# Optimization experiments

Measured on AMD Instinct MI355X. Metric: run time of the kernel, lower is better.

## Reference

```python
import jax, jax.numpy as jnp
import numpy as np

TAU = 1.0
ITERATIONS = 5
NEG = -1e9  # effectively -inf for masked softmax; exp underflows to exactly 0

B, N, M = 128, 512, 512


def setup_inputs() -> dict:
    key = jax.random.key(0)
    k1, k2, k3 = jax.random.split(key, 3)
    logits = jax.random.normal(k1, (B, N, M), dtype=jnp.float32)
    free_agents_num = jax.random.randint(k2, (B,), 0, M, dtype=jnp.int32)
    tasks_num = jax.random.randint(k3, (B,), 0, M, dtype=jnp.int32)
    return {"logits": logits, "free_agents_num": free_agents_num, "tasks_num": tasks_num}


def reference(logits, free_agents_num, tasks_num):
    # step is None in the original default path -> tau = self.tau
    b, n, m = logits.shape
    row_valid = jnp.arange(n)[None, :] < free_agents_num[:, None]  # [B, N]
    col_valid = jnp.arange(m)[None, :] < tasks_num[:, None]        # [B, M]
    mask = row_valid[:, :, None] & col_valid[:, None, :]           # [B, N, M]
    maskf = mask.astype(logits.dtype)

    x = logits / TAU
    for _ in range(ITERATIONS):
        # torch dim=1 on the [na, nt] slice == axis 2 here (over tasks)
        x = jax.nn.softmax(jnp.where(mask, x, NEG), axis=2) * maskf
        # torch dim=0 on the slice == axis 1 here (over agents)
        x = jax.nn.softmax(jnp.where(mask, x, NEG), axis=1) * maskf
    return x
```

## Files before the change

kernel.cpp:

```cpp
#include <hip/hip_runtime.h>

static constexpr int NB = 128;
static constexpr int NN = 512;
static constexpr int NM = 512;
static constexpr int STRIPS = 8;
static constexpr int NTHREADS = 256;
static constexpr int NITER = 5;
static constexpr int PSZ = NB * NM * STRIPS;


__device__ __forceinline__ float wave_sum(float v) {
#pragma unroll
    for (int off = 32; off >= 1; off >>= 1) v += __shfl_xor(v, off, 64);
    return v;
}

__global__ __launch_bounds__(NTHREADS, 4)
void k0_init(const float* __restrict__ logits, const int* __restrict__ nfree,
             const int* __restrict__ ntask, float* __restrict__ X,
             float* __restrict__ part0)
{
    const int b = blockIdx.x & (NB - 1);
    const int s = blockIdx.x >> 7;
    const int na = nfree[b], nt = ntask[b];
    const int tid = threadIdx.x, wv = tid >> 6, lane = tid & 63;
    float* __restrict__ Xb       = X + (size_t)b * NN * NM;
    const float* __restrict__ Lb = logits + (size_t)b * NN * NM;

    __shared__ __align__(16) float red[4][NM];

    const int m0 = lane * 4, m1 = 256 + lane * 4;
    const bool a0 = (m0 < nt), a1 = (m1 < nt);
    float msk[8];
#pragma unroll
    for (int k = 0; k < 8; ++k)
        msk[k] = (((k < 4) ? m0 + k : m1 + k - 4) < nt) ? 1.f : 0.f;

    const int rstart = s + 8 * wv;
    float ca[8];
#pragma unroll
    for (int k = 0; k < 8; ++k) ca[k] = 0.f;

    int r = rstart;
    for (; r < na; r += 32) {
        float e[8];
#pragma unroll
        for (int k = 0; k < 8; ++k) e[k] = 0.f;
        if (a0) {
            const float4 x = *(const float4*)(Lb + (size_t)r * NM + m0);
            e[0] = msk[0] * __expf(x.x); e[1] = msk[1] * __expf(x.y);
            e[2] = msk[2] * __expf(x.z); e[3] = msk[3] * __expf(x.w);
        }
        if (a1) {
            const float4 x = *(const float4*)(Lb + (size_t)r * NM + m1);
            e[4] = msk[4] * __expf(x.x); e[5] = msk[5] * __expf(x.y);
            e[6] = msk[6] * __expf(x.z); e[7] = msk[7] * __expf(x.w);
        }
        const float sum = wave_sum(((e[0] + e[1]) + (e[2] + e[3])) +
                                   ((e[4] + e[5]) + (e[6] + e[7])));
        const float invr = 1.0f / sum;
        float4 o0 = make_float4(0.f, 0.f, 0.f, 0.f), o1 = o0;
        if (a0) {
            o0 = make_float4(msk[0] * __expf(e[0] * invr), msk[1] * __expf(e[1] * invr),
                             msk[2] * __expf(e[2] * invr), msk[3] * __expf(e[3] * invr));
            ca[0] += o0.x; ca[1] += o0.y; ca[2] += o0.z; ca[3] += o0.w;
        }
        if (a1) {
            o1 = make_float4(msk[4] * __expf(e[4] * invr), msk[5] * __expf(e[5] * invr),
                             msk[6] * __expf(e[6] * invr), msk[7] * __expf(e[7] * invr));
            ca[4] += o1.x; ca[5] += o1.y; ca[6] += o1.z; ca[7] += o1.w;
        }
        *(float4*)(Xb + (size_t)r * NM + m0) = o0;
        *(float4*)(Xb + (size_t)r * NM + m1) = o1;
    }
    const float4 z4 = make_float4(0.f, 0.f, 0.f, 0.f);
    for (; r < NN; r += 32) {
        *(float4*)(Xb + (size_t)r * NM + m0) = z4;
        *(float4*)(Xb + (size_t)r * NM + m1) = z4;
    }

    *(float4*)&red[wv][m0] = make_float4(ca[0], ca[1], ca[2], ca[3]);
    *(float4*)&red[wv][m1] = make_float4(ca[4], ca[5], ca[6], ca[7]);
    __syncthreads();
    {
        float* pb = part0 + (size_t)b * NM * STRIPS;
        const int c = tid * 2;
        pb[(size_t)c * STRIPS + s]       = (red[0][c] + red[1][c]) + (red[2][c] + red[3][c]);
        pb[(size_t)(c + 1) * STRIPS + s] = (red[0][c + 1] + red[1][c + 1]) + (red[2][c + 1] + red[3][c + 1]);
    }
}

__global__ __launch_bounds__(NTHREADS, 4)
void k1_cr(const int* __restrict__ nfree, const int* __restrict__ ntask,
           float* __restrict__ X, const float* __restrict__ ps,
           float* __restrict__ pd)
{
    const int b = blockIdx.x & (NB - 1);
    const int s = blockIdx.x >> 7;
    const int na = nfree[b], nt = ntask[b];
    const int tid = threadIdx.x, wv = tid >> 6, lane = tid & 63;
    float* __restrict__ Xb = X + (size_t)b * NN * NM;

    __shared__ __align__(16) float red[4][NM];
    __shared__ __align__(16) float csh[NM];

    const float* psb = ps + (size_t)b * NM * STRIPS;
    {
        const int c = tid * 2;
        const float4* p0 = (const float4*)(psb + (size_t)c * STRIPS);
        float4 u = p0[0], v = p0[1];
        csh[c] = ((u.x + u.y) + (u.z + u.w)) + ((v.x + v.y) + (v.z + v.w));
        const float4* p1 = (const float4*)(psb + (size_t)(c + 1) * STRIPS);
        u = p1[0]; v = p1[1];
        csh[c + 1] = ((u.x + u.y) + (u.z + u.w)) + ((v.x + v.y) + (v.z + v.w));
    }
    __syncthreads();

    const int m0 = lane * 4, m1 = 256 + lane * 4;
    const bool a0 = (m0 < nt), a1 = (m1 < nt);
    float msk[8], inv[8];
#pragma unroll
    for (int k = 0; k < 8; ++k) {
        const int m = (k < 4) ? m0 + k : m1 + k - 4;
        msk[k] = (m < nt) ? 1.f : 0.f;
        inv[k] = (m < nt) ? 1.0f / csh[m] : 0.f;
    }
    const int rstart = s + 8 * wv;
    float cn[8];
#pragma unroll
    for (int k = 0; k < 8; ++k) cn[k] = 0.f;

    for (int r = rstart; r < na; r += 32) {
        float ez[8];
#pragma unroll
        for (int k = 0; k < 8; ++k) ez[k] = 0.f;
        if (a0) {
            const float4 y = *(const float4*)(Xb + (size_t)r * NM + m0);
            ez[0] = msk[0] * __expf(y.x * inv[0]); ez[1] = msk[1] * __expf(y.y * inv[1]);
            ez[2] = msk[2] * __expf(y.z * inv[2]); ez[3] = msk[3] * __expf(y.w * inv[3]);
        }
        if (a1) {
            const float4 y = *(const float4*)(Xb + (size_t)r * NM + m1);
            ez[4] = msk[4] * __expf(y.x * inv[4]); ez[5] = msk[5] * __expf(y.y * inv[5]);
            ez[6] = msk[6] * __expf(y.z * inv[6]); ez[7] = msk[7] * __expf(y.w * inv[7]);
        }
        const float sum = wave_sum(((ez[0] + ez[1]) + (ez[2] + ez[3])) +
                                   ((ez[4] + ez[5]) + (ez[6] + ez[7])));
        const float invr = 1.0f / sum;
        if (a0) {
            const float4 o = make_float4(
                msk[0] * __expf(ez[0] * invr), msk[1] * __expf(ez[1] * invr),
                msk[2] * __expf(ez[2] * invr), msk[3] * __expf(ez[3] * invr));
            *(float4*)(Xb + (size_t)r * NM + m0) = o;
            cn[0] += o.x; cn[1] += o.y; cn[2] += o.z; cn[3] += o.w;
        }
        if (a1) {
            const float4 o = make_float4(
                msk[4] * __expf(ez[4] * invr), msk[5] * __expf(ez[5] * invr),
                msk[6] * __expf(ez[6] * invr), msk[7] * __expf(ez[7] * invr));
            *(float4*)(Xb + (size_t)r * NM + m1) = o;
            cn[4] += o.x; cn[5] += o.y; cn[6] += o.z; cn[7] += o.w;
        }
    }

    *(float4*)&red[wv][m0] = make_float4(cn[0], cn[1], cn[2], cn[3]);
    *(float4*)&red[wv][m1] = make_float4(cn[4], cn[5], cn[6], cn[7]);
    __syncthreads();
    {
        float* pdb = pd + (size_t)b * NM * STRIPS;
        const int c = tid * 2;
        pdb[(size_t)c * STRIPS + s]       = (red[0][c] + red[1][c]) + (red[2][c] + red[3][c]);
        pdb[(size_t)(c + 1) * STRIPS + s] = (red[0][c + 1] + red[1][c + 1]) + (red[2][c + 1] + red[3][c + 1]);
    }
}

__global__ __launch_bounds__(NTHREADS, 4)
void k2_fin(const int* __restrict__ nfree, const int* __restrict__ ntask,
            float* __restrict__ X, const float* __restrict__ ps)
{
    const int b = blockIdx.x & (NB - 1);
    const int s = blockIdx.x >> 7;
    const int na = nfree[b], nt = ntask[b];
    const int tid = threadIdx.x, wv = tid >> 6, lane = tid & 63;
    float* __restrict__ Xb = X + (size_t)b * NN * NM;

    __shared__ __align__(16) float csh[NM];
    const float* psb = ps + (size_t)b * NM * STRIPS;
    {
        const int c = tid * 2;
        const float4* p0 = (const float4*)(psb + (size_t)c * STRIPS);
        float4 u = p0[0], v = p0[1];
        csh[c] = ((u.x + u.y) + (u.z + u.w)) + ((v.x + v.y) + (v.z + v.w));
        const float4* p1 = (const float4*)(psb + (size_t)(c + 1) * STRIPS);
        u = p1[0]; v = p1[1];
        csh[c + 1] = ((u.x + u.y) + (u.z + u.w)) + ((v.x + v.y) + (v.z + v.w));
    }
    __syncthreads();

    const int m0 = lane * 4, m1 = 256 + lane * 4;
    const bool a0 = (m0 < nt), a1 = (m1 < nt);
    float inv[8];
#pragma unroll
    for (int k = 0; k < 8; ++k) {
        const int m = (k < 4) ? m0 + k : m1 + k - 4;
        inv[k] = (m < nt) ? 1.0f / csh[m] : 0.f;
    }
    const int rstart = s + 8 * wv;
    for (int r = rstart; r < na; r += 32) {
        if (a0) {
            const float4 y = *(const float4*)(Xb + (size_t)r * NM + m0);
            *(float4*)(Xb + (size_t)r * NM + m0) =
                make_float4(y.x * inv[0], y.y * inv[1], y.z * inv[2], y.w * inv[3]);
        }
        if (a1) {
            const float4 y = *(const float4*)(Xb + (size_t)r * NM + m1);
            *(float4*)(Xb + (size_t)r * NM + m1) =
                make_float4(y.x * inv[4], y.y * inv[5], y.z * inv[6], y.w * inv[7]);
        }
    }
}

extern "C" void kernel_launch(void* const* d_in, const int* in_sizes, int n_in,
                              void* d_out, int out_size, void* d_ws, size_t ws_size,
                              hipStream_t stream)
{
    (void)in_sizes; (void)n_in; (void)out_size; (void)ws_size;
    const float* logits = (const float*)d_in[0];
    const int* nfree    = (const int*)d_in[1];
    const int* ntask    = (const int*)d_in[2];
    float* X  = (float*)d_out;
    float* p0 = (float*)d_ws;
    float* p1 = p0 + PSZ;

    const dim3 grid(NB * STRIPS), block(NTHREADS);
    hipLaunchKernelGGL(k0_init, grid, block, 0, stream, logits, nfree, ntask, X, p0);
    const float* src = p0;
    float* dst = p1;
    for (int it = 0; it < NITER - 1; ++it) {
        hipLaunchKernelGGL(k1_cr, grid, block, 0, stream, nfree, ntask, X, src, dst);
        const float* t = src; src = dst; dst = (float*)t;
    }
    hipLaunchKernelGGL(k2_fin, grid, block, 0, stream, nfree, ntask, X, src);
}
```

Measured before the change: 351.7 us.

## Fuse all Sinkhorn passes into one cooperative kernel with grid-wide syncs

Merges the init, iterative column/row normalization, and final scaling kernels into a single cooperative launch that uses grid.sync between passes, with fallback to the multi-launch path if co-residency is not possible. The aim is to remove per-launch overhead and inter-kernel gaps. It requires all 1024 blocks to be co-resident, and grid barriers carry their own cost.

```diff
diff --git a/kernel.cpp b/kernel.cpp
--- a/kernel.cpp
+++ b/kernel.cpp
@@ -1,4 +1,7 @@
 #include <hip/hip_runtime.h>
+#include <hip/hip_cooperative_groups.h>
+
+namespace cg = cooperative_groups;
 
 static constexpr int NB = 128;
 static constexpr int NN = 512;
@@ -15,20 +18,11 @@
     return v;
 }
 
-__global__ __launch_bounds__(NTHREADS, 4)
-void k0_init(const float* __restrict__ logits, const int* __restrict__ nfree,
-             const int* __restrict__ ntask, float* __restrict__ X,
-             float* __restrict__ part0)
-{
-    const int b = blockIdx.x & (NB - 1);
-    const int s = blockIdx.x >> 7;
-    const int na = nfree[b], nt = ntask[b];
-    const int tid = threadIdx.x, wv = tid >> 6, lane = tid & 63;
-    float* __restrict__ Xb       = X + (size_t)b * NN * NM;
-    const float* __restrict__ Lb = logits + (size_t)b * NN * NM;
-
-    __shared__ __align__(16) float red[4][NM];
-
+
+__device__ __forceinline__ void body_init(
+    const float* __restrict__ Lb, float* __restrict__ Xb, float* __restrict__ pb,
+    int s, int na, int nt, int tid, int wv, int lane, float (&red)[4][NM])
+{
     const int m0 = lane * 4, m1 = 256 + lane * 4;
     const bool a0 = (m0 < nt), a1 = (m1 < nt);
     float msk[8];
@@ -83,37 +77,30 @@
     *(float4*)&red[wv][m1] = make_float4(ca[4], ca[5], ca[6], ca[7]);
     __syncthreads();
     {
-        float* pb = part0 + (size_t)b * NM * STRIPS;
         const int c = tid * 2;
         pb[(size_t)c * STRIPS + s]       = (red[0][c] + red[1][c]) + (red[2][c] + red[3][c]);
         pb[(size_t)(c + 1) * STRIPS + s] = (red[0][c + 1] + red[1][c + 1]) + (red[2][c + 1] + red[3][c + 1]);
     }
 }
 
-__global__ __launch_bounds__(NTHREADS, 4)
-void k1_cr(const int* __restrict__ nfree, const int* __restrict__ ntask,
-           float* __restrict__ X, const float* __restrict__ ps,
-           float* __restrict__ pd)
-{
-    const int b = blockIdx.x & (NB - 1);
-    const int s = blockIdx.x >> 7;
-    const int na = nfree[b], nt = ntask[b];
-    const int tid = threadIdx.x, wv = tid >> 6, lane = tid & 63;
-    float* __restrict__ Xb = X + (size_t)b * NN * NM;
-
-    __shared__ __align__(16) float red[4][NM];
-    __shared__ __align__(16) float csh[NM];
-
-    const float* psb = ps + (size_t)b * NM * STRIPS;
-    {
-        const int c = tid * 2;
-        const float4* p0 = (const float4*)(psb + (size_t)c * STRIPS);
-        float4 u = p0[0], v = p0[1];
-        csh[c] = ((u.x + u.y) + (u.z + u.w)) + ((v.x + v.y) + (v.z + v.w));
-        const float4* p1 = (const float4*)(psb + (size_t)(c + 1) * STRIPS);
-        u = p1[0]; v = p1[1];
-        csh[c + 1] = ((u.x + u.y) + (u.z + u.w)) + ((v.x + v.y) + (v.z + v.w));
-    }
+__device__ __forceinline__ void gather_colsums(
+    const float* __restrict__ psb, int tid, float (&csh)[NM])
+{
+    const int c = tid * 2;
+    const float4* p0 = (const float4*)(psb + (size_t)c * STRIPS);
+    float4 u = p0[0], v = p0[1];
+    csh[c] = ((u.x + u.y) + (u.z + u.w)) + ((v.x + v.y) + (v.z + v.w));
+    const float4* p1 = (const float4*)(psb + (size_t)(c + 1) * STRIPS);
+    u = p1[0]; v = p1[1];
+    csh[c + 1] = ((u.x + u.y) + (u.z + u.w)) + ((v.x + v.y) + (v.z + v.w));
+}
+
+__device__ __forceinline__ void body_cr(
+    float* __restrict__ Xb, const float* __restrict__ psb, float* __restrict__ pdb,
+    int s, int na, int nt, int tid, int wv, int lane,
+    float (&red)[4][NM], float (&csh)[NM])
+{
+    gather_colsums(psb, tid, csh);
     __syncthreads();
 
     const int m0 = lane * 4, m1 = 256 + lane * 4;
@@ -167,57 +154,107 @@
     *(float4*)&red[wv][m1] = make_float4(cn[4], cn[5], cn[6], cn[7]);
     __syncthreads();
     {
-        float* pdb = pd + (size_t)b * NM * STRIPS;
         const int c = tid * 2;
         pdb[(size_t)c * STRIPS + s]       = (red[0][c] + red[1][c]) + (red[2][c] + red[3][c]);
         pdb[(size_t)(c + 1) * STRIPS + s] = (red[0][c + 1] + red[1][c + 1]) + (red[2][c + 1] + red[3][c + 1]);
     }
 }
 
+__device__ __forceinline__ void body_fin(
+    float* __restrict__ Xb, const float* __restrict__ psb,
+    int s, int na, int nt, int tid, int wv, int lane, float (&csh)[NM])
+{
+    gather_colsums(psb, tid, csh);
+    __syncthreads();
+
+    const int m0 = lane * 4, m1 = 256 + lane * 4;
+    const bool a0 = (m0 < nt), a1 = (m1 < nt);
+    float inv[8];
+#pragma unroll
+    for (int k = 0; k < 8; ++k) {
+        const int m = (k < 4) ? m0 + k : m1 + k - 4;
+        inv[k] = (m < nt) ? 1.0f / csh[m] : 0.f;
+    }
+    const int rstart = s + 8 * wv;
+    for (int r = rstart; r < na; r += 32) {
+        if (a0) {
+            const float4 y = *(const float4*)(Xb + (size_t)r * NM + m0);
+            *(float4*)(Xb + (size_t)r * NM + m0) =
+                make_float4(y.x * inv[0], y.y * inv[1], y.z * inv[2], y.w * inv[3]);
+        }
+        if (a1) {
+            const float4 y = *(const float4*)(Xb + (size_t)r * NM + m1);
+            *(float4*)(Xb + (size_t)r * NM + m1) =
+                make_float4(y.x * inv[4], y.y * inv[5], y.z * inv[6], y.w * inv[7]);
+        }
+    }
+}
+
+
 __global__ __launch_bounds__(NTHREADS, 4)
-void k2_fin(const int* __restrict__ nfree, const int* __restrict__ ntask,
-            float* __restrict__ X, const float* __restrict__ ps)
-{
+void gs_coop(const float* __restrict__ logits, const int* __restrict__ nfree,
+             const int* __restrict__ ntask, float* __restrict__ X,
+             float* __restrict__ part)
+{
+    cg::grid_group grid = cg::this_grid();
     const int b = blockIdx.x & (NB - 1);
     const int s = blockIdx.x >> 7;
     const int na = nfree[b], nt = ntask[b];
     const int tid = threadIdx.x, wv = tid >> 6, lane = tid & 63;
-    float* __restrict__ Xb = X + (size_t)b * NN * NM;
-
+
+    float* __restrict__ Xb       = X + (size_t)b * NN * NM;
+    const float* __restrict__ Lb = logits + (size_t)b * NN * NM;
+    float* const pbase = part + (size_t)b * NM * STRIPS;
+
+    __shared__ __align__(16) float red[4][NM];
     __shared__ __align__(16) float csh[NM];
-    const float* psb = ps + (size_t)b * NM * STRIPS;
-    {
-        const int c = tid * 2;
-        const float4* p0 = (const float4*)(psb + (size_t)c * STRIPS);
-        float4 u = p0[0], v = p0[1];
-        csh[c] = ((u.x + u.y) + (u.z + u.w)) + ((v.x + v.y) + (v.z + v.w));
-        const float4* p1 = (const float4*)(psb + (size_t)(c + 1) * STRIPS);
-        u = p1[0]; v = p1[1];
-        csh[c + 1] = ((u.x + u.y) + (u.z + u.w)) + ((v.x + v.y) + (v.z + v.w));
-    }
-    __syncthreads();
-
-    const int m0 = lane * 4, m1 = 256 + lane * 4;
-    const bool a0 = (m0 < nt), a1 = (m1 < nt);
-    float inv[8];
-#pragma unroll
-    for (int k = 0; k < 8; ++k) {
-        const int m = (k < 4) ? m0 + k : m1 + k - 4;
-        inv[k] = (m < nt) ? 1.0f / csh[m] : 0.f;
-    }
-    const int rstart = s + 8 * wv;
-    for (int r = rstart; r < na; r += 32) {
-        if (a0) {
-            const float4 y = *(const float4*)(Xb + (size_t)r * NM + m0);
-            *(float4*)(Xb + (size_t)r * NM + m0) =
-                make_float4(y.x * inv[0], y.y * inv[1], y.z * inv[2], y.w * inv[3]);
-        }
-        if (a1) {
-            const float4 y = *(const float4*)(Xb + (size_t)r * NM + m1);
-            *(float4*)(Xb + (size_t)r * NM + m1) =
-                make_float4(y.x * inv[4], y.y * inv[5], y.z * inv[6], y.w * inv[7]);
-        }
-    }
+
+    body_init(Lb, Xb, pbase, s, na, nt, tid, wv, lane, red);
+    grid.sync();
+
+    for (int it = 0; it < NITER - 1; ++it) {
+        const float* psb = pbase + ((it & 1) ? PSZ : 0);
+        float* pdb       = pbase + ((it & 1) ? 0 : PSZ);
+        body_cr(Xb, psb, pdb, s, na, nt, tid, wv, lane, red, csh);
+        grid.sync();
+    }
+    body_fin(Xb, pbase, s, na, nt, tid, wv, lane, csh);
+}
+
+
+__global__ __launch_bounds__(NTHREADS, 4)
+void k0_init(const float* __restrict__ logits, const int* __restrict__ nfree,
+             const int* __restrict__ ntask, float* __restrict__ X,
+             float* __restrict__ part0)
+{
+    const int b = blockIdx.x & (NB - 1), s = blockIdx.x >> 7;
+    const int tid = threadIdx.x, wv = tid >> 6, lane = tid & 63;
+    __shared__ __align__(16) float red[4][NM];
+    body_init(logits + (size_t)b * NN * NM, X + (size_t)b * NN * NM,
+              part0 + (size_t)b * NM * STRIPS, s, nfree[b], ntask[b], tid, wv, lane, red);
+}
+
+__global__ __launch_bounds__(NTHREADS, 4)
+void k1_cr(const int* __restrict__ nfree, const int* __restrict__ ntask,
+           float* __restrict__ X, const float* __restrict__ ps, float* __restrict__ pd)
+{
+    const int b = blockIdx.x & (NB - 1), s = blockIdx.x >> 7;
+    const int tid = threadIdx.x, wv = tid >> 6, lane = tid & 63;
+    __shared__ __align__(16) float red[4][NM];
+    __shared__ __align__(16) float csh[NM];
+    body_cr(X + (size_t)b * NN * NM, ps + (size_t)b * NM * STRIPS,
+            pd + (size_t)b * NM * STRIPS, s, nfree[b], ntask[b], tid, wv, lane, red, csh);
+}
+
+__global__ __launch_bounds__(NTHREADS, 4)
+void k2_fin(const int* __restrict__ nfree, const int* __restrict__ ntask,
+            float* __restrict__ X, const float* __restrict__ ps)
+{
+    const int b = blockIdx.x & (NB - 1), s = blockIdx.x >> 7;
+    const int tid = threadIdx.x, wv = tid >> 6, lane = tid & 63;
+    __shared__ __align__(16) float csh[NM];
+    body_fin(X + (size_t)b * NN * NM, ps + (size_t)b * NM * STRIPS,
+             s, nfree[b], ntask[b], tid, wv, lane, csh);
 }
 
 extern "C" void kernel_launch(void* const* d_in, const int* in_sizes, int n_in,
@@ -228,17 +265,36 @@
     const float* logits = (const float*)d_in[0];
     const int* nfree    = (const int*)d_in[1];
     const int* ntask    = (const int*)d_in[2];
-    float* X  = (float*)d_out;
-    float* p0 = (float*)d_ws;
-    float* p1 = p0 + PSZ;
-
-    const dim3 grid(NB * STRIPS), block(NTHREADS);
-    hipLaunchKernelGGL(k0_init, grid, block, 0, stream, logits, nfree, ntask, X, p0);
-    const float* src = p0;
-    float* dst = p1;
-    for (int it = 0; it < NITER - 1; ++it) {
-        hipLaunchKernelGGL(k1_cr, grid, block, 0, stream, nfree, ntask, X, src, dst);
-        const float* t = src; src = dst; dst = (float*)t;
-    }
-    hipLaunchKernelGGL(k2_fin, grid, block, 0, stream, nfree, ntask, X, src);
-}
+    float* X    = (float*)d_out;
+    float* part = (float*)d_ws;
+
+    bool coop_ok = false;
+    {
+        int dev = 0;
+        if (hipGetDevice(&dev) == hipSuccess) {
+            int num_cu = 0, max_blk = 0;
+            if (hipDeviceGetAttribute(&num_cu, hipDeviceAttributeMultiprocessorCount, dev) == hipSuccess &&
+                hipOccupancyMaxActiveBlocksPerMultiprocessor(&max_blk, gs_coop, NTHREADS, 0) == hipSuccess)
+                coop_ok = ((long)max_blk * num_cu >= NB * STRIPS);
+        }
+    }
+
+    if (coop_ok) {
+        void* args[] = {(void*)&logits, (void*)&nfree, (void*)&ntask,
+                        (void*)&X, (void*)&part};
+        coop_ok = (hipSuccess == hipLaunchCooperativeKernel(
+                       (const void*)gs_coop, dim3(NB * STRIPS), dim3(NTHREADS),
+                       args, 0, stream));
+    }
+    if (!coop_ok) {
+        const dim3 grid(NB * STRIPS), block(NTHREADS);
+        hipLaunchKernelGGL(k0_init, grid, block, 0, stream, logits, nfree, ntask, X, part);
+        const float* src = part;
+        float* dst = part + PSZ;
+        for (int it = 0; it < NITER - 1; ++it) {
+            hipLaunchKernelGGL(k1_cr, grid, block, 0, stream, nfree, ntask, X, src, dst);
+            const float* t = src; src = dst; dst = (float*)t;
+        }
+        hipLaunchKernelGGL(k2_fin, grid, block, 0, stream, nfree, ntask, X, src);
+    }
+}
```

Result: no change. 349.5 us (-0.6%).
